# Performance work log

Hardware: AMD Instinct MI355X
Metric: run time of the kernel (lower is better)

Reference implementation:

```python
import jax, jax.numpy as jnp
import numpy as np

B, L, D_MODEL, H = 2, 2048, 1024, 16
HD = D_MODEL // H  # head dim = 64


def setup_inputs() -> dict:
    key = jax.random.key(0)
    ks = jax.random.split(key, 11)
    s = 1.0 / np.sqrt(D_MODEL)
    inp = {
        "Q": jax.random.normal(ks[0], (B, L, D_MODEL), jnp.float32),
        "K": jax.random.normal(ks[1], (B, L, D_MODEL), jnp.float32),
        "V": jax.random.normal(ks[2], (B, L, D_MODEL), jnp.float32),
        "Wq": jax.random.normal(ks[3], (D_MODEL, D_MODEL), jnp.float32) * s,
        "bq": jnp.zeros((D_MODEL,), jnp.float32),
        "Wk": jax.random.normal(ks[4], (D_MODEL, D_MODEL), jnp.float32) * s,
        "bk": jnp.zeros((D_MODEL,), jnp.float32),
        "Wv": jax.random.normal(ks[5], (D_MODEL, D_MODEL), jnp.float32) * s,
        "bv": jnp.zeros((D_MODEL,), jnp.float32),
        "Wo": jax.random.normal(ks[6], (D_MODEL, D_MODEL), jnp.float32) * s,
        "bo": jnp.zeros((D_MODEL,), jnp.float32),
    }
    return inp


def _split_heads(x):
    # [B, L, H*D] -> [B, H, L, D]
    return x.reshape(B, L, H, HD).transpose(0, 2, 1, 3)


def reference(Q, K, V, Wq, bq, Wk, bk, Wv, bv, Wo, bo):
    q = _split_heads(Q @ Wq.T + bq)
    k = _split_heads(K @ Wk.T + bk)
    v = _split_heads(V @ Wv.T + bv)
    scale = 1.0 / jnp.sqrt(jnp.asarray(HD, q.dtype))
    # full [B, H, L, L] score matrix, as in the original bmm->softmax->bmm
    scores = jnp.einsum("bhqd,bhkd->bhqk", q, k) * scale
    attn = jax.nn.softmax(scores, axis=-1)
    o = jnp.einsum("bhqk,bhkd->bhqd", attn, v)
    o = o.transpose(0, 2, 1, 3).reshape(B, L, D_MODEL)  # concat heads
    return o @ Wo.T + bo
```

## Files before the change

### kernel.cpp

```cpp
#include <hip/hip_runtime.h>
#include <math.h>
#include <stdint.h>

typedef __bf16 bf16_t;
typedef __attribute__((ext_vector_type(2))) __bf16 bf16x2;
typedef __attribute__((ext_vector_type(8))) __bf16 bf16x8;
typedef __attribute__((ext_vector_type(4))) float f32x4;
typedef __attribute__((ext_vector_type(16))) float f32x16;
typedef __attribute__((address_space(1))) unsigned int gu32;
typedef __attribute__((address_space(3))) unsigned int lu32;

#define MFMA16(a, b, c) __builtin_amdgcn_mfma_f32_16x16x32_bf16((a), (b), (c), 0, 0, 0)
#define MFMA32(a, b, c) __builtin_amdgcn_mfma_f32_32x32x16_bf16((a), (b), (c), 0, 0, 0)

__device__ __forceinline__ void gll16(const void* g, void* l) {
    __builtin_amdgcn_global_load_lds((const gu32*)(uintptr_t)g,
                                     (lu32*)(uintptr_t)l, 16, 0, 0);
}

__device__ __forceinline__ bf16x8 ld_frag68(const bf16_t* p) {
    union { bf16x8 v; uint2 u[2]; } r;
    r.u[0] = *(const uint2*)p;
    r.u[1] = *(const uint2*)(p + 4);
    return r.v;
}

__global__ __launch_bounds__(256) void convert_all(
    const float* __restrict__ Q, const float* __restrict__ K, const float* __restrict__ V,
    const float* __restrict__ Wq, const float* __restrict__ Wk, const float* __restrict__ Wv,
    const float* __restrict__ Wo, bf16_t* __restrict__ dst) {
    size_t e0 = (size_t)blockIdx.x * 2048;
    const float* src; size_t off;
    if (e0 < 4194304)       { src = Q;  off = e0; }
    else if (e0 < 8388608)  { src = K;  off = e0 - 4194304; }
    else if (e0 < 12582912) { src = V;  off = e0 - 8388608; }
    else if (e0 < 13631488) { src = Wq; off = e0 - 12582912; }
    else if (e0 < 14680064) { src = Wk; off = e0 - 13631488; }
    else if (e0 < 15728640) { src = Wv; off = e0 - 14680064; }
    else                    { src = Wo; off = e0 - 15728640; }
#pragma unroll
    for (int p = 0; p < 2; ++p) {
        int t = p * 1024 + threadIdx.x * 4;
        float4 v = *(const float4*)(src + off + t);
        union { ushort4 u; bf16_t h[4]; } pk;
        pk.h[0] = (bf16_t)v.x; pk.h[1] = (bf16_t)v.y;
        pk.h[2] = (bf16_t)v.z; pk.h[3] = (bf16_t)v.w;
        *(ushort4*)(dst + e0 + t) = pk.u;
    }
}

__global__ __launch_bounds__(256) void qkv_gemm(
    const bf16_t* __restrict__ Qb, const bf16_t* __restrict__ Kb, const bf16_t* __restrict__ Vb,
    const bf16_t* __restrict__ Wqb, const bf16_t* __restrict__ Wkb, const bf16_t* __restrict__ Wvb,
    const float* __restrict__ bq, const float* __restrict__ bk, const float* __restrict__ bv,
    bf16_t* __restrict__ qo, bf16_t* __restrict__ ko, bf16_t* __restrict__ vT) {
    constexpr int Kdim = 1024, N = 1024;
    __shared__ __attribute__((aligned(16))) bf16_t smem[4 * 128 * 64];

    const int tid = threadIdx.x, wave = tid >> 6, lane = tid & 63;
    const int z = blockIdx.z;
    const bf16_t* A = (z == 0) ? Qb : (z == 1) ? Kb : Vb;
    const bf16_t* W = (z == 0) ? Wqb : (z == 1) ? Wkb : Wvb;
    const float* bias = (z == 0) ? bq : (z == 1) ? bk : bv;
    const int bm = blockIdx.x * 128, bn = blockIdx.y * 128;
    const int l16 = lane & 15, quad = lane >> 4;
    const int wm = (wave >> 1) * 64, wn = (wave & 1) * 64;
    const int grow = lane >> 3;
    const int gcol = (((lane & 7) ^ grow)) * 8;
    const int rsw = l16 & 7;

    f32x4 acc[4][4] = {};

    auto stage = [&](int k0, bf16_t* As, bf16_t* Bs) {
#pragma unroll
        for (int j = 0; j < 4; ++j) {
            int chunk = wave * 4 + j;
            int row = chunk * 8 + grow;
            gll16(A + (size_t)(bm + row) * Kdim + k0 + gcol, As + chunk * 512);
            gll16(W + (size_t)(bn + row) * Kdim + k0 + gcol, Bs + chunk * 512);
        }
    };
    auto compute = [&](const bf16_t* As, const bf16_t* Bs) {
#pragma unroll
        for (int ks = 0; ks < 64; ks += 32) {
            const int sl = ((ks >> 3) + quad);
            const int so = (sl ^ rsw) * 8;
            bf16x8 af[4], bf[4];
#pragma unroll
            for (int i = 0; i < 4; ++i)
                af[i] = *(const bf16x8*)&As[(wm + i * 16 + l16) * 64 + so];
#pragma unroll
            for (int i = 0; i < 4; ++i)
                bf[i] = *(const bf16x8*)&Bs[(wn + i * 16 + l16) * 64 + so];
#pragma unroll
            for (int i = 0; i < 4; ++i)
#pragma unroll
                for (int j = 0; j < 4; ++j)
                    acc[i][j] = MFMA16(af[i], bf[j], acc[i][j]);
        }
    };

    stage(0, smem, smem + 8192);
    asm volatile("s_waitcnt vmcnt(0)" ::: "memory");
    __builtin_amdgcn_s_barrier();
    int cur = 0;
    for (int t = 0; t < 15; ++t) {
        bf16_t* nb = smem + (cur ^ 1) * 16384;
        stage((t + 1) * 64, nb, nb + 8192);
        bf16_t* cb = smem + cur * 16384;
        compute(cb, cb + 8192);
        asm volatile("s_waitcnt vmcnt(0)" ::: "memory");
        __builtin_amdgcn_s_barrier();
        cur ^= 1;
    }
    {
        bf16_t* cb = smem + cur * 16384;
        compute(cb, cb + 8192);
    }

    if (z < 2) {
        bf16_t* outp = (z == 0) ? qo : ko;
        const float sc = (z == 0) ? 0.18033688011112042f : 1.0f;
        constexpr int RST = 132;
#pragma unroll
        for (int p = 0; p < 2; ++p) {
            __syncthreads();
            if ((wave >> 1) == p) {
#pragma unroll
                for (int mi = 0; mi < 4; ++mi)
#pragma unroll
                    for (int nj = 0; nj < 4; ++nj) {
                        int col = wn + nj * 16 + l16;
                        float bv_ = bias[bn + col];
#pragma unroll
                        for (int r = 0; r < 4; ++r) {
                            int rp = mi * 16 + quad * 4 + r;
                            smem[rp * RST + col] = (bf16_t)((acc[mi][nj][r] + bv_) * sc);
                        }
                    }
            }
            __syncthreads();
            int rp = tid >> 2;
            int cb2 = (tid & 3) * 32;
            int row = bm + p * 64 + rp;
#pragma unroll
            for (int j = 0; j < 4; ++j) {
                uint2 lo = *(const uint2*)&smem[rp * RST + cb2 + j * 8];
                uint2 hi = *(const uint2*)&smem[rp * RST + cb2 + j * 8 + 4];
                *(uint4*)&outp[(size_t)row * N + bn + cb2 + j * 8] =
                    make_uint4(lo.x, lo.y, hi.x, hi.y);
            }
        }
    } else {
#pragma unroll
        for (int mi = 0; mi < 4; ++mi)
#pragma unroll
            for (int nj = 0; nj < 4; ++nj) {
                int col = bn + wn + nj * 16 + l16;
                int h = col >> 6, d = col & 63;
                float bv_ = bias[col];
                int row0 = bm + wm + mi * 16 + quad * 4;
                int bb = row0 >> 11, l = row0 & 2047;
                int lb = (l & ~12) | ((l & 4) << 1) | ((l & 8) >> 1);
                union { ushort4 u; bf16_t h4[4]; } pk;
#pragma unroll
                for (int r = 0; r < 4; ++r) pk.h4[r] = (bf16_t)(acc[mi][nj][r] + bv_);
                *(ushort4*)&vT[(((size_t)bb * 16 + h) * 64 + d) * 2048 + lb] = pk.u;
            }
    }
}

__global__ __launch_bounds__(256) void out_gemm(const bf16_t* __restrict__ A,
                                                const bf16_t* __restrict__ W,
                                                const float* __restrict__ bias,
                                                float* __restrict__ out) {
    constexpr int Kdim = 1024, N = 1024;
    __shared__ __attribute__((aligned(16))) bf16_t smem[2 * 12288];
    const int tid = threadIdx.x, wave = tid >> 6, lane = tid & 63;
    const int bm = blockIdx.x * 64, bn = blockIdx.y * 128;
    const int l16 = lane & 15, quad = lane >> 4;
    const int wm = (wave >> 1) * 32, wn = (wave & 1) * 64;
    const int grow = lane >> 3;
    const int gcol = (((lane & 7) ^ grow)) * 8;
    const int rsw = l16 & 7;
    f32x4 acc[2][4] = {};

    auto stage = [&](int k0, bf16_t* As, bf16_t* Bs) {
#pragma unroll
        for (int j = 0; j < 2; ++j) {
            int chunk = wave * 2 + j;
            int row = chunk * 8 + grow;
            gll16(A + (size_t)(bm + row) * Kdim + k0 + gcol, As + chunk * 512);
        }
#pragma unroll
        for (int j = 0; j < 4; ++j) {
            int chunk = wave * 4 + j;
            int row = chunk * 8 + grow;
            gll16(W + (size_t)(bn + row) * Kdim + k0 + gcol, Bs + chunk * 512);
        }
    };
    auto compute = [&](const bf16_t* As, const bf16_t* Bs) {
#pragma unroll
        for (int ks = 0; ks < 64; ks += 32) {
            const int so0 = ((((ks >> 3) + quad)) ^ rsw) * 8;
            bf16x8 af[2], bf[4];
#pragma unroll
            for (int i = 0; i < 2; ++i)
                af[i] = *(const bf16x8*)&As[(wm + i * 16 + l16) * 64 + so0];
#pragma unroll
            for (int i = 0; i < 4; ++i)
                bf[i] = *(const bf16x8*)&Bs[(wn + i * 16 + l16) * 64 + so0];
#pragma unroll
            for (int i = 0; i < 2; ++i)
#pragma unroll
                for (int j = 0; j < 4; ++j)
                    acc[i][j] = MFMA16(af[i], bf[j], acc[i][j]);
        }
    };

    stage(0, smem, smem + 4096);
    asm volatile("s_waitcnt vmcnt(0)" ::: "memory");
    __builtin_amdgcn_s_barrier();
    int cur = 0;
    for (int t = 0; t < 15; ++t) {
        bf16_t* nb = smem + (cur ^ 1) * 12288;
        stage((t + 1) * 64, nb, nb + 4096);
        bf16_t* cb = smem + cur * 12288;
        compute(cb, cb + 4096);
        asm volatile("s_waitcnt vmcnt(0)" ::: "memory");
        __builtin_amdgcn_s_barrier();
        cur ^= 1;
    }
    {
        bf16_t* cb = smem + cur * 12288;
        compute(cb, cb + 4096);
    }

#pragma unroll
    for (int mi = 0; mi < 2; ++mi)
#pragma unroll
        for (int nj = 0; nj < 4; ++nj) {
            int col = bn + wn + nj * 16 + l16;
            float bv_ = bias[col];
#pragma unroll
            for (int r = 0; r < 4; ++r) {
                int row = bm + wm + mi * 16 + quad * 4 + r;
                out[(size_t)row * N + col] = acc[mi][nj][r] + bv_;
            }
        }
}

__global__ __launch_bounds__(256, 4) void attn6(const bf16_t* __restrict__ qo,
                                                const bf16_t* __restrict__ ko,
                                                const bf16_t* __restrict__ vT,
                                                bf16_t* __restrict__ Op,
                                                float* __restrict__ lpp) {
    constexpr int L = 2048, D = 1024, ST = 68;
    constexpr int BUF = 2 * 64 * ST;
    __shared__ __attribute__((aligned(16))) bf16_t smem[2 * BUF];

    const int tid = threadIdx.x, wave = tid >> 6, lane = tid & 63;
    const int l31 = lane & 31, hi = lane >> 5;
    const int b = blockIdx.x >> 4, h = blockIdx.x & 15;
    const int q0 = blockIdx.y * 128;
    const int split = blockIdx.z;
    bf16_t* Opart = Op + (size_t)split * 4194304;
    float* lpart = lpp + split * 65536;

    const int rloc = tid >> 2, cg = tid & 3;
    const bf16_t* kbase = ko + ((size_t)b * L + rloc) * D + h * 64 + cg * 16;
    const bf16_t* vbase = vT + (((size_t)b * 16 + h) * 64 + rloc) * L + cg * 16;

    bf16x8 qf[4];
    {
        const bf16_t* qptr = qo + ((size_t)b * L + q0 + wave * 32 + l31) * D + h * 64 + hi * 8;
#pragma unroll
        for (int ks = 0; ks < 4; ++ks) qf[ks] = *(const bf16x8*)(qptr + ks * 16);
    }

    f32x16 o0{}, o1{};
    float lpl = 0.f;

    const int kt0 = split * 16, kt1 = kt0 + 16;

    uint4 ka, kc, va, vc;
    auto gload = [&](int kt) {
        const size_t koff = (size_t)(kt * 64) * D;
        const int voff = kt * 64;
        ka = *(const uint4*)(kbase + koff);
        kc = *(const uint4*)(kbase + koff + 8);
        va = *(const uint4*)(vbase + voff);
        vc = *(const uint4*)(vbase + voff + 8);
    };
    auto swrite = [&](bf16_t* buf) {
        bf16_t* kd = &buf[rloc * ST + cg * 16];
        bf16_t* vd = &buf[64 * ST + rloc * ST + cg * 16];
        *(uint2*)(kd + 0)  = make_uint2(ka.x, ka.y);
        *(uint2*)(kd + 4)  = make_uint2(ka.z, ka.w);
        *(uint2*)(kd + 8)  = make_uint2(kc.x, kc.y);
        *(uint2*)(kd + 12) = make_uint2(kc.z, kc.w);
        *(uint2*)(vd + 0)  = make_uint2(va.x, va.y);
        *(uint2*)(vd + 4)  = make_uint2(va.z, va.w);
        *(uint2*)(vd + 8)  = make_uint2(vc.x, vc.y);
        *(uint2*)(vd + 12) = make_uint2(vc.z, vc.w);
    };

    gload(kt0);
    swrite(smem);
    gload(kt0 + 1 < kt1 ? kt0 + 1 : kt1 - 1);
    asm volatile("s_waitcnt lgkmcnt(0)" ::: "memory");
    __builtin_amdgcn_s_barrier();

    int cur = 0;
    for (int kt = kt0; kt < kt1; ++kt) {
        swrite(smem + (cur ^ 1) * BUF);
        gload(kt + 2 < kt1 ? kt + 2 : kt1 - 1);
        const bf16_t* ksm = smem + cur * BUF;
        const bf16_t* vsm = ksm + 64 * ST;

        f32x16 s0{}, s1{};
        __builtin_amdgcn_s_setprio(1);
#pragma unroll
        for (int ks = 0; ks < 4; ++ks) {
            bf16x8 k0 = ld_frag68(&ksm[l31 * ST + ks * 16 + hi * 8]);
            bf16x8 k1 = ld_frag68(&ksm[(32 + l31) * ST + ks * 16 + hi * 8]);
            s0 = MFMA32(k0, qf[ks], s0);
            s1 = MFMA32(k1, qf[ks], s1);
        }
        __builtin_amdgcn_s_setprio(0);

#pragma unroll
        for (int t = 0; t < 4; ++t) {
            union { bf16x8 v; bf16_t e[8]; } pf;
#pragma unroll
            for (int j = 0; j < 8; ++j) {
                float sv = (t < 2) ? s0[(t & 1) * 8 + j] : s1[(t & 1) * 8 + j];
                float p = __builtin_amdgcn_exp2f(sv);
                lpl += p;
                pf.e[j] = (bf16_t)p;
            }
            bf16x8 v0 = ld_frag68(&vsm[l31 * ST + t * 16 + hi * 8]);
            bf16x8 v1 = ld_frag68(&vsm[(32 + l31) * ST + t * 16 + hi * 8]);
            __builtin_amdgcn_s_setprio(1);
            o0 = MFMA32(v0, pf.v, o0);
            o1 = MFMA32(v1, pf.v, o1);
            __builtin_amdgcn_s_setprio(0);
        }

        asm volatile("s_waitcnt lgkmcnt(0)" ::: "memory");
        __builtin_amdgcn_s_barrier();
        cur ^= 1;
    }

    lpl += __shfl_xor(lpl, 32, 64);
    if (hi == 0)
        lpart[((size_t)b * 16 + h) * 2048 + q0 + wave * 32 + l31] = lpl;

    __syncthreads();
    bf16_t* ew = smem + wave * (32 * ST);
#pragma unroll
    for (int r = 0; r < 16; r += 2) {
        int d = (r & 3) + 8 * (r >> 2) + 4 * hi;
        *(bf16x2*)&ew[l31 * ST + d] = bf16x2{(bf16_t)o0[r], (bf16_t)o0[r + 1]};
        *(bf16x2*)&ew[l31 * ST + 32 + d] = bf16x2{(bf16_t)o1[r], (bf16_t)o1[r + 1]};
    }
#pragma unroll
    for (int p = 0; p < 4; ++p) {
        int rr = p * 8 + (lane >> 3);
        int cc = (lane & 7) * 8;
        uint2 lo = *(const uint2*)&ew[rr * ST + cc];
        uint2 hi2 = *(const uint2*)&ew[rr * ST + cc + 4];
        *(uint4*)&Opart[((size_t)b * L + q0 + wave * 32 + rr) * D + h * 64 + cc] =
            make_uint4(lo.x, lo.y, hi2.x, hi2.y);
    }
}

__global__ __launch_bounds__(256) void combine(const bf16_t* __restrict__ Op,
                                               const float* __restrict__ lpp,
                                               bf16_t* __restrict__ Ob) {
    const size_t c = (size_t)blockIdx.x * 256 + threadIdx.x;
    const int bl = (int)(c >> 7);
    const int h = ((int)c >> 3) & 15;
    const int bb = bl >> 11, l = bl & 2047;
    const int li = (bb * 16 + h) * 2048 + l;
    const float inv = 1.f / (lpp[li] + lpp[65536 + li]);
    union { uint4 u; bf16_t h8[8]; } a, b, o;
    a.u = *(const uint4*)(Op + c * 8);
    b.u = *(const uint4*)(Op + 4194304 + c * 8);
#pragma unroll
    for (int i = 0; i < 8; ++i)
        o.h8[i] = (bf16_t)(((float)a.h8[i] + (float)b.h8[i]) * inv);
    *(uint4*)(Ob + c * 8) = o.u;
}

extern "C" void kernel_launch(void* const* d_in, const int* in_sizes, int n_in,
                              void* d_out, int out_size, void* d_ws, size_t ws_size,
                              hipStream_t stream) {
    const float* Q  = (const float*)d_in[0];
    const float* Kx = (const float*)d_in[1];
    const float* V  = (const float*)d_in[2];
    const float* Wq = (const float*)d_in[3];
    const float* bq = (const float*)d_in[4];
    const float* Wk = (const float*)d_in[5];
    const float* bk = (const float*)d_in[6];
    const float* Wv = (const float*)d_in[7];
    const float* bv = (const float*)d_in[8];
    const float* Wo = (const float*)d_in[9];
    const float* bo = (const float*)d_in[10];

    bf16_t* ws0 = (bf16_t*)d_ws;
    bf16_t* Qb  = ws0;
    bf16_t* Kb  = ws0 + 4194304;
    bf16_t* Vb  = ws0 + 8388608;
    bf16_t* Wqb = ws0 + 12582912;
    bf16_t* Wkb = ws0 + 13631488;
    bf16_t* Wvb = ws0 + 14680064;
    bf16_t* Wob = ws0 + 15728640;
    bf16_t* vT  = ws0 + 16777216;
    bf16_t* Op  = Qb;
    bf16_t* Obf = Vb;
    float*  lpp = (float*)Wqb;
    bf16_t* qo = (bf16_t*)d_out;
    bf16_t* ko = qo + 4194304;

    convert_all<<<8192, 256, 0, stream>>>(Q, Kx, V, Wq, Wk, Wv, Wo, ws0);
    qkv_gemm<<<dim3(32, 8, 3), 256, 0, stream>>>(Qb, Kb, Vb, Wqb, Wkb, Wvb,
                                                 bq, bk, bv, qo, ko, vT);
    attn6<<<dim3(32, 16, 2), 256, 0, stream>>>(qo, ko, vT, Op, lpp);
    combine<<<2048, 256, 0, stream>>>(Op, lpp, Obf);
    out_gemm<<<dim3(64, 8), 256, 0, stream>>>(Obf, Wob, bo, (float*)d_out);
}
```

Measured before the change: 222.7 us.

## Process two query tiles per attention block to reuse K/V shared-memory loads

Each attention workgroup now handles 256 query rows instead of 128. Each wave holds two sets of Q fragments and accumulators and reuses every K and V fragment read from LDS for both query groups. The grid is halved and the launch bound drops to 2 blocks per SM. The goal is to halve K/V global and LDS traffic per unit of work, at the cost of higher register pressure, lower occupancy and only 512 blocks in the grid.

```diff
diff --git a/kernel.cpp b/kernel.cpp
--- a/kernel.cpp
+++ b/kernel.cpp
@@ -250,7 +250,7 @@
         }
 }
 
-__global__ __launch_bounds__(256, 4) void attn6(const bf16_t* __restrict__ qo,
+__global__ __launch_bounds__(256, 2) void attn8(const bf16_t* __restrict__ qo,
                                                 const bf16_t* __restrict__ ko,
                                                 const bf16_t* __restrict__ vT,
                                                 bf16_t* __restrict__ Op,
@@ -262,7 +262,7 @@
     const int tid = threadIdx.x, wave = tid >> 6, lane = tid & 63;
     const int l31 = lane & 31, hi = lane >> 5;
     const int b = blockIdx.x >> 4, h = blockIdx.x & 15;
-    const int q0 = blockIdx.y * 128;
+    const int q0 = blockIdx.y * 256;
     const int split = blockIdx.z;
     bf16_t* Opart = Op + (size_t)split * 4194304;
     float* lpart = lpp + split * 65536;
@@ -271,15 +271,19 @@
     const bf16_t* kbase = ko + ((size_t)b * L + rloc) * D + h * 64 + cg * 16;
     const bf16_t* vbase = vT + (((size_t)b * 16 + h) * 64 + rloc) * L + cg * 16;
 
-    bf16x8 qf[4];
+    bf16x8 qfa[4], qfb[4];
     {
-        const bf16_t* qptr = qo + ((size_t)b * L + q0 + wave * 32 + l31) * D + h * 64 + hi * 8;
-#pragma unroll
-        for (int ks = 0; ks < 4; ++ks) qf[ks] = *(const bf16x8*)(qptr + ks * 16);
-    }
-
-    f32x16 o0{}, o1{};
-    float lpl = 0.f;
+        const bf16_t* qa = qo + ((size_t)b * L + q0 + wave * 32 + l31) * D + h * 64 + hi * 8;
+        const bf16_t* qb2 = qa + (size_t)128 * D;
+#pragma unroll
+        for (int ks = 0; ks < 4; ++ks) {
+            qfa[ks] = *(const bf16x8*)(qa + ks * 16);
+            qfb[ks] = *(const bf16x8*)(qb2 + ks * 16);
+        }
+    }
+
+    f32x16 o0a{}, o1a{}, o0b{}, o1b{};
+    float lpla = 0.f, lplb = 0.f;
 
     const int kt0 = split * 16, kt1 = kt0 + 16;
 
@@ -318,32 +322,39 @@
         const bf16_t* ksm = smem + cur * BUF;
         const bf16_t* vsm = ksm + 64 * ST;
 
-        f32x16 s0{}, s1{};
+        f32x16 s0a{}, s1a{}, s0b{}, s1b{};
         __builtin_amdgcn_s_setprio(1);
 #pragma unroll
         for (int ks = 0; ks < 4; ++ks) {
             bf16x8 k0 = ld_frag68(&ksm[l31 * ST + ks * 16 + hi * 8]);
             bf16x8 k1 = ld_frag68(&ksm[(32 + l31) * ST + ks * 16 + hi * 8]);
-            s0 = MFMA32(k0, qf[ks], s0);
-            s1 = MFMA32(k1, qf[ks], s1);
+            s0a = MFMA32(k0, qfa[ks], s0a);
+            s1a = MFMA32(k1, qfa[ks], s1a);
+            s0b = MFMA32(k0, qfb[ks], s0b);
+            s1b = MFMA32(k1, qfb[ks], s1b);
         }
         __builtin_amdgcn_s_setprio(0);
 
 #pragma unroll
         for (int t = 0; t < 4; ++t) {
-            union { bf16x8 v; bf16_t e[8]; } pf;
+            union { bf16x8 v; bf16_t e[8]; } pfa, pfb;
 #pragma unroll
             for (int j = 0; j < 8; ++j) {
-                float sv = (t < 2) ? s0[(t & 1) * 8 + j] : s1[(t & 1) * 8 + j];
-                float p = __builtin_amdgcn_exp2f(sv);
-                lpl += p;
-                pf.e[j] = (bf16_t)p;
+                float sva = (t < 2) ? s0a[(t & 1) * 8 + j] : s1a[(t & 1) * 8 + j];
+                float svb = (t < 2) ? s0b[(t & 1) * 8 + j] : s1b[(t & 1) * 8 + j];
+                float pa = __builtin_amdgcn_exp2f(sva);
+                float pb = __builtin_amdgcn_exp2f(svb);
+                lpla += pa; lplb += pb;
+                pfa.e[j] = (bf16_t)pa;
+                pfb.e[j] = (bf16_t)pb;
             }
             bf16x8 v0 = ld_frag68(&vsm[l31 * ST + t * 16 + hi * 8]);
             bf16x8 v1 = ld_frag68(&vsm[(32 + l31) * ST + t * 16 + hi * 8]);
             __builtin_amdgcn_s_setprio(1);
-            o0 = MFMA32(v0, pf.v, o0);
-            o1 = MFMA32(v1, pf.v, o1);
+            o0a = MFMA32(v0, pfa.v, o0a);
+            o1a = MFMA32(v1, pfa.v, o1a);
+            o0b = MFMA32(v0, pfb.v, o0b);
+            o1b = MFMA32(v1, pfb.v, o1b);
             __builtin_amdgcn_s_setprio(0);
         }
 
@@ -352,17 +363,20 @@
         cur ^= 1;
     }
 
-    lpl += __shfl_xor(lpl, 32, 64);
-    if (hi == 0)
-        lpart[((size_t)b * 16 + h) * 2048 + q0 + wave * 32 + l31] = lpl;
+    lpla += __shfl_xor(lpla, 32, 64);
+    lplb += __shfl_xor(lplb, 32, 64);
+    if (hi == 0) {
+        lpart[((size_t)b * 16 + h) * 2048 + q0 + wave * 32 + l31] = lpla;
+        lpart[((size_t)b * 16 + h) * 2048 + q0 + 128 + wave * 32 + l31] = lplb;
+    }
 
     __syncthreads();
     bf16_t* ew = smem + wave * (32 * ST);
 #pragma unroll
     for (int r = 0; r < 16; r += 2) {
         int d = (r & 3) + 8 * (r >> 2) + 4 * hi;
-        *(bf16x2*)&ew[l31 * ST + d] = bf16x2{(bf16_t)o0[r], (bf16_t)o0[r + 1]};
-        *(bf16x2*)&ew[l31 * ST + 32 + d] = bf16x2{(bf16_t)o1[r], (bf16_t)o1[r + 1]};
+        *(bf16x2*)&ew[l31 * ST + d] = bf16x2{(bf16_t)o0a[r], (bf16_t)o0a[r + 1]};
+        *(bf16x2*)&ew[l31 * ST + 32 + d] = bf16x2{(bf16_t)o1a[r], (bf16_t)o1a[r + 1]};
     }
 #pragma unroll
     for (int p = 0; p < 4; ++p) {
@@ -371,6 +385,21 @@
         uint2 lo = *(const uint2*)&ew[rr * ST + cc];
         uint2 hi2 = *(const uint2*)&ew[rr * ST + cc + 4];
         *(uint4*)&Opart[((size_t)b * L + q0 + wave * 32 + rr) * D + h * 64 + cc] =
+            make_uint4(lo.x, lo.y, hi2.x, hi2.y);
+    }
+#pragma unroll
+    for (int r = 0; r < 16; r += 2) {
+        int d = (r & 3) + 8 * (r >> 2) + 4 * hi;
+        *(bf16x2*)&ew[l31 * ST + d] = bf16x2{(bf16_t)o0b[r], (bf16_t)o0b[r + 1]};
+        *(bf16x2*)&ew[l31 * ST + 32 + d] = bf16x2{(bf16_t)o1b[r], (bf16_t)o1b[r + 1]};
+    }
+#pragma unroll
+    for (int p = 0; p < 4; ++p) {
+        int rr = p * 8 + (lane >> 3);
+        int cc = (lane & 7) * 8;
+        uint2 lo = *(const uint2*)&ew[rr * ST + cc];
+        uint2 hi2 = *(const uint2*)&ew[rr * ST + cc + 4];
+        *(uint4*)&Opart[((size_t)b * L + q0 + 128 + wave * 32 + rr) * D + h * 64 + cc] =
             make_uint4(lo.x, lo.y, hi2.x, hi2.y);
     }
 }
@@ -426,7 +455,7 @@
     convert_all<<<8192, 256, 0, stream>>>(Q, Kx, V, Wq, Wk, Wv, Wo, ws0);
     qkv_gemm<<<dim3(32, 8, 3), 256, 0, stream>>>(Qb, Kb, Vb, Wqb, Wkb, Wvb,
                                                  bq, bk, bv, qo, ko, vT);
-    attn6<<<dim3(32, 16, 2), 256, 0, stream>>>(qo, ko, vT, Op, lpp);
+    attn8<<<dim3(32, 8, 2), 256, 0, stream>>>(qo, ko, vT, Op, lpp);
     combine<<<2048, 256, 0, stream>>>(Op, lpp, Obf);
     out_gemm<<<dim3(64, 8), 256, 0, stream>>>(Obf, Wob, bo, (float*)d_out);
 }
```

After: 217.6 us. -2.3%, faster.
